# Optimization experiments

Measured on AMD Instinct MI355X. Metric: run time of the kernel, lower is better.

The kernel has to match this reference:

```python
import jax, jax.numpy as jnp
import numpy as np

EPS = 1.1920929e-07  # torch RMSNorm default eps = float32 finfo eps

def rms_norm(x, w):
    return x * jax.lax.rsqrt(jnp.mean(x * x, axis=-1, keepdims=True) + EPS) * w

def setup_inputs() -> dict:
    key = jax.random.key(0)
    ks = jax.random.split(key, 10)
    B, C, H, W = 8, 64, 48, 48
    E = C  # embed_dim = query_dim = key_dim = value_dim
    q = jax.random.normal(ks[0], (B, C, H, W), jnp.float32)
    k = jax.random.normal(ks[1], (B, C, H, W), jnp.float32)
    v = jax.random.normal(ks[2], (B, C, H, W), jnp.float32)
    s = 1.0 / np.sqrt(E)
    conv_w = jax.random.normal(ks[3], (C, C, 3, 3), jnp.float32) * (1.0 / np.sqrt(C * 9))
    nq_w = jnp.ones((E,), jnp.float32)
    nk_w = jnp.ones((E,), jnp.float32)
    wq = jax.random.normal(ks[4], (E, E), jnp.float32) * s
    bq = jax.random.normal(ks[5], (E,), jnp.float32) * 0.01
    wk = jax.random.normal(ks[6], (E, E), jnp.float32) * s
    bk = jax.random.normal(ks[7], (E,), jnp.float32) * 0.01
    return {"q": q, "k": k, "v": v, "conv_w": conv_w, "nq_w": nq_w,
            "nk_w": nk_w, "wq": wq, "bq": bq, "wk": wk, "bk": bk}

def reference(q, k, v, conv_w, nq_w, nk_w, wq, bq, wk, bk):
    B, C, H, W = q.shape
    num_heads = 4
    head_dim = C // num_heads
    # conv2d 3x3, stride 1, same padding, no bias
    qc = jax.lax.conv_general_dilated(
        q, conv_w, window_strides=(1, 1), padding='SAME',
        dimension_numbers=('NCHW', 'OIHW', 'NCHW'))
    # b c h w -> b (h w) c
    qs = qc.reshape(B, C, H * W).transpose(0, 2, 1)
    ksq = k.reshape(B, C, -1).transpose(0, 2, 1)
    vsq = v.reshape(B, C, -1).transpose(0, 2, 1)
    # RMSNorm on q and k (norm_v output feeds MHA value path whose output is discarded)
    qn = rms_norm(qs, nq_w)
    kn = rms_norm(ksq, nk_w)
    # MHA projections (q scaled by 1/sqrt(head_dim) as in torch)
    qp = (qn @ wq.T + bq) * (1.0 / np.sqrt(head_dim))
    kp = ksq_p = kn @ wk.T + bk
    Sq, Sk = qp.shape[1], kp.shape[1]
    qh = qp.reshape(B, Sq, num_heads, head_dim)
    kh = kp.reshape(B, Sk, num_heads, head_dim)
    scores = jnp.einsum('bihd,bjhd->bhij', qh, kh)
    attn = jax.nn.softmax(scores, axis=-1)
    # average_attn_weights=True -> mean over heads
    attn_avg = jnp.mean(attn, axis=1)  # [b, i, j]
    # custom output: weighted sum over RAW (un-normed, unprojected) value
    out = jnp.einsum('bij,bjd->bid', attn_avg, vsq)
    return out
```

## Files before the change

### kernel.cpp

```cpp
#include <hip/hip_runtime.h>
#include <hip/hip_bf16.h>

namespace {
constexpr int kB = 8;
constexpr int kC = 64;
constexpr int kH = 48;
constexpr int kW = 48;
constexpr int kS = kH * kW;
constexpr float kEps = 1.1920929e-07f;
constexpr float kQScale = 0.25f * 1.4426950408889634f;
}

typedef __attribute__((ext_vector_type(8))) short short8;
typedef __attribute__((ext_vector_type(4))) float f32x4;

__device__ __forceinline__ short f2bf(float x) {
  unsigned u = __float_as_uint(x);
  u += 0x7fffu + ((u >> 16) & 1u);
  return (short)(u >> 16);
}
__device__ __forceinline__ float bf2f(short s) {
  return __uint_as_float(((unsigned)(unsigned short)s) << 16);
}
__device__ __forceinline__ float fexp2(float x) {
  return __builtin_amdgcn_exp2f(x);
}

__global__ __launch_bounds__(256) void fused_prep(
    const float* __restrict__ q, const float* __restrict__ k,
    const float* __restrict__ v, const float* __restrict__ wq,
    const float* __restrict__ wk, const float* __restrict__ conv_w,
    short* __restrict__ qt, short* __restrict__ kt, short* __restrict__ vq,
    short* __restrict__ wqb3, short* __restrict__ wkb3, short* __restrict__ wt3) {
  const int blk = blockIdx.x;
  if (blk < 576) {
    __shared__ float tile[64][65];
    const int zz = blk / 36;
    const int bx = blk % 36;
    const int b = zz >> 1;
    const float* src = (zz & 1) ? k : q;
    short* dst = (zz & 1) ? kt : qt;
    const int s0 = bx * 64;
    const int tx = threadIdx.x & 63;
    const int ty = threadIdx.x >> 6;
#pragma unroll
    for (int r = 0; r < 16; ++r) {
      int c = r * 4 + ty;
      tile[c][tx] = src[((size_t)b * kC + c) * kS + s0 + tx];
    }
    __syncthreads();
#pragma unroll
    for (int r = 0; r < 16; ++r) {
      int s = r * 4 + ty;
      dst[((size_t)b * kS + s0 + s) * kC + tx] = f2bf(tile[tx][s]);
    }
  } else if (blk < 1152) {
    int g = (blk - 576) * 256 + threadIdx.x;
    int bb = g / 18432;
    int rem = g - bb * 18432;
    int jseg = rem >> 8;
    int sub = rem & 255;
    int d = sub >> 6;
    int Lq = sub & 63;
    const float* src = v + ((size_t)(bb * 64 + d * 16 + (Lq & 15))) * kS
                         + jseg * 32 + (Lq >> 4) * 8;
    float4 x0 = *reinterpret_cast<const float4*>(src);
    float4 x1 = *reinterpret_cast<const float4*>(src + 4);
    short8 o;
    o[0] = f2bf(x0.x); o[1] = f2bf(x0.y); o[2] = f2bf(x0.z); o[3] = f2bf(x0.w);
    o[4] = f2bf(x1.x); o[5] = f2bf(x1.y); o[6] = f2bf(x1.z); o[7] = f2bf(x1.w);
    *reinterpret_cast<short8*>(vq + (size_t)g * 8) = o;
  } else {
    int idx = (blk - 1152) * 256 + threadIdx.x;
    if (idx < 4096) {
      int j = idx & 7, Lw = (idx >> 3) & 63, slab = idx >> 9;
      int nt = slab & 3, kh = slab >> 2;
      int e = nt * 16 + (Lw & 15), c = kh * 32 + (Lw >> 4) * 8 + j;
      wqb3[idx] = f2bf(wq[e * 64 + c]);
    } else if (idx < 8192) {
      int i2 = idx - 4096;
      int j = i2 & 7, Lw = (i2 >> 3) & 63, slab = i2 >> 9;
      int nt = slab & 3, kh = slab >> 2;
      int e = nt * 16 + (Lw & 15), c = kh * 32 + (Lw >> 4) * 8 + j;
      wkb3[i2] = f2bf(wk[e * 64 + c]);
    } else {
      int i3 = idx - 8192;
      int j = i3 & 7, Lw = (i3 >> 3) & 63, slab = i3 >> 9;
      int nt = slab & 3, kh = (slab >> 2) & 1, tap = slab >> 3;
      int co = nt * 16 + (Lw & 15), ci = kh * 32 + (Lw >> 4) * 8 + j;
      wt3[i3] = f2bf(conv_w[co * 576 + ci * 9 + tap]);
    }
  }
}

__global__ __launch_bounds__(256) void fused_qk_gemm(
    const short* __restrict__ qt, const short* __restrict__ kt,
    const short* __restrict__ wt3, const short* __restrict__ wqb3,
    const short* __restrict__ wkb3,
    const float* __restrict__ nq_w, const float* __restrict__ nk_w,
    const float* __restrict__ bq, const float* __restrict__ bk,
    short* __restrict__ qp, short* __restrict__ kq) {
  __shared__ __align__(16) short Qs[164][72];
  __shared__ __align__(16) short ln[4][16][80];
  const int blk = blockIdx.x;
  const int t = threadIdx.x;
  const int ws = t >> 6;
  const int L = t & 63;
  const int quad = L >> 4;
  const int l16 = L & 15;
  const short8 zero8 = {0, 0, 0, 0, 0, 0, 0, 0};

  if (blk < 288) {
    const int b = blk / 36;
    const int S0 = (blk % 36) * 64;
    const int sBase = S0 + ws * 16;
    const int s = sBase + l16;
    const int h = s / kW, w = s % kW;

    const short* qtb = qt + (size_t)b * kS * kC;
#pragma unroll
    for (int it = 0; it < 6; ++it) {
      int idx = it * 256 + t;
      if (idx < 164 * 8) {
        int r = idx >> 3, sg = idx & 7;
        int srow = S0 - 49 + r;
        srow = srow < 0 ? 0 : (srow >= kS ? kS - 1 : srow);
        *reinterpret_cast<int4*>(&Qs[r][sg * 8]) =
            *reinterpret_cast<const int4*>(qtb + (size_t)srow * kC + sg * 8);
      }
    }
    __syncthreads();

    const int baseLocal = ws * 16 + l16 + 49;
    f32x4 acc[4] = {{0.f, 0.f, 0.f, 0.f}, {0.f, 0.f, 0.f, 0.f},
                    {0.f, 0.f, 0.f, 0.f}, {0.f, 0.f, 0.f, 0.f}};
#pragma unroll
    for (int tap = 0; tap < 9; ++tap) {
      const int dh = tap / 3 - 1, dw = tap % 3 - 1;
      const bool valid = (unsigned)(h + dh) < (unsigned)kH &&
                         (unsigned)(w + dw) < (unsigned)kW;
      const int local = baseLocal + dh * kW + dw;
#pragma unroll
      for (int kh = 0; kh < 2; ++kh) {
        short8 af = *reinterpret_cast<const short8*>(&Qs[local][kh * 32 + quad * 8]);
        af = valid ? af : zero8;
        const short* wb = wt3 + ((tap * 2 + kh) * 4) * 512 + L * 8;
#pragma unroll
        for (int nt = 0; nt < 4; ++nt) {
          short8 bf = *reinterpret_cast<const short8*>(wb + nt * 512);
          acc[nt] = __builtin_amdgcn_mfma_f32_16x16x32_bf16(af, bf, acc[nt], 0, 0, 0);
        }
      }
    }
    float rstd[4];
#pragma unroll
    for (int reg = 0; reg < 4; ++reg) {
      float pr = acc[0][reg] * acc[0][reg] + acc[1][reg] * acc[1][reg]
               + acc[2][reg] * acc[2][reg] + acc[3][reg] * acc[3][reg];
      pr += __shfl_xor(pr, 1, 64);
      pr += __shfl_xor(pr, 2, 64);
      pr += __shfl_xor(pr, 4, 64);
      pr += __shfl_xor(pr, 8, 64);
      rstd[reg] = rsqrtf(pr * (1.0f / kC) + kEps);
    }
#pragma unroll
    for (int nt = 0; nt < 4; ++nt) {
      float g = nq_w[nt * 16 + l16];
#pragma unroll
      for (int reg = 0; reg < 4; ++reg) {
        ln[ws][quad * 4 + reg][nt * 16 + l16] = f2bf(acc[nt][reg] * rstd[reg] * g);
      }
    }
    __syncthreads();
    f32x4 acc2[4] = {{0.f, 0.f, 0.f, 0.f}, {0.f, 0.f, 0.f, 0.f},
                     {0.f, 0.f, 0.f, 0.f}, {0.f, 0.f, 0.f, 0.f}};
#pragma unroll
    for (int kh = 0; kh < 2; ++kh) {
      short8 af = *reinterpret_cast<const short8*>(&ln[ws][l16][kh * 32 + quad * 8]);
      const short* wb = wqb3 + (kh * 4) * 512 + L * 8;
#pragma unroll
      for (int nt = 0; nt < 4; ++nt) {
        short8 bf = *reinterpret_cast<const short8*>(wb + nt * 512);
        acc2[nt] = __builtin_amdgcn_mfma_f32_16x16x32_bf16(af, bf, acc2[nt], 0, 0, 0);
      }
    }
#pragma unroll
    for (int nt = 0; nt < 4; ++nt) {
      const int e = nt * 16 + l16;
      float bias = bq[e];
#pragma unroll
      for (int reg = 0; reg < 4; ++reg) {
        qp[((size_t)b * kS + sBase + quad * 4 + reg) * kC + e] =
            f2bf((acc2[nt][reg] + bias) * kQScale);
      }
    }
  } else {
    const int idx = blk - 288;
    const int b = idx / 36;
    const int S0 = (idx % 36) * 64;
    const int sBase = S0 + ws * 16;

    const short* ktb = kt + ((size_t)b * kS + S0) * kC;
#pragma unroll
    for (int it = 0; it < 2; ++it) {
      int r = it * 32 + (t >> 3), sg = t & 7;
      *reinterpret_cast<int4*>(&Qs[r][sg * 8]) =
          *reinterpret_cast<const int4*>(ktb + (size_t)r * kC + sg * 8);
    }
    __syncthreads();

    short8 af0 = *reinterpret_cast<const short8*>(&Qs[ws * 16 + l16][quad * 8]);
    short8 af1 = *reinterpret_cast<const short8*>(&Qs[ws * 16 + l16][32 + quad * 8]);

    float xs[16];
#pragma unroll
    for (int j = 0; j < 8; ++j) { xs[j] = bf2f(af0[j]); xs[8 + j] = bf2f(af1[j]); }
    float sum = 0.f;
#pragma unroll
    for (int j = 0; j < 16; ++j) sum = fmaf(xs[j], xs[j], sum);
    sum += __shfl_xor(sum, 16, 64);
    sum += __shfl_xor(sum, 32, 64);
    float rstd = rsqrtf(sum * (1.0f / kC) + kEps);

    const float* n0 = nk_w + quad * 8;
#pragma unroll
    for (int j = 0; j < 8; ++j) {
      af0[j] = f2bf(xs[j] * rstd * n0[j]);
      af1[j] = f2bf(xs[8 + j] * rstd * n0[32 + j]);
    }

    f32x4 acc[4] = {{0.f, 0.f, 0.f, 0.f}, {0.f, 0.f, 0.f, 0.f},
                    {0.f, 0.f, 0.f, 0.f}, {0.f, 0.f, 0.f, 0.f}};
#pragma unroll
    for (int nt = 0; nt < 4; ++nt) {
      short8 bf0 = *reinterpret_cast<const short8*>(
          wkb3 + (0 * 4 + nt) * 512 + L * 8);
      short8 bf1 = *reinterpret_cast<const short8*>(
          wkb3 + (1 * 4 + nt) * 512 + L * 8);
      acc[nt] = __builtin_amdgcn_mfma_f32_16x16x32_bf16(af0, bf0, acc[nt], 0, 0, 0);
      acc[nt] = __builtin_amdgcn_mfma_f32_16x16x32_bf16(af1, bf1, acc[nt], 0, 0, 0);
    }
    short* kqb = kq + (size_t)b * 147456;
#pragma unroll
    for (int nt = 0; nt < 4; ++nt) {
      const int e = nt * 16 + l16;
      const int hp = nt >> 1;
      const int quadp = ((nt & 1) << 1) | (l16 >> 3);
      const int elem = l16 & 7;
      float bias = bk[e];
#pragma unroll
      for (int reg = 0; reg < 4; ++reg) {
        int s = sBase + quad * 4 + reg;
        int jseg = s >> 5, jrow = s & 31;
        int c = (jrow >> 2) & 1;
        int l16p = ((jrow >> 3) << 2) | (jrow & 3);
        kqb[((((size_t)jseg * 2 + hp) * 2 + c) * 64 + quadp * 16 + l16p) * 8 + elem] =
            f2bf(acc[nt][reg] + bias);
      }
    }
  }
}

#define LOADT(K0, K1, V0, V1, V2, V3, JT)                                      \
  do {                                                                         \
    const short* kb_ = kbase + (size_t)(JT) * 4096;                            \
    const short* vb_ = vbase + (size_t)(JT) * 4096;                            \
    K0 = *reinterpret_cast<const short8*>(kb_);                                \
    K1 = *reinterpret_cast<const short8*>(kb_ + 512);                          \
    V0 = *reinterpret_cast<const short8*>(vb_);                                \
    V1 = *reinterpret_cast<const short8*>(vb_ + 512);                          \
    V2 = *reinterpret_cast<const short8*>(vb_ + 1024);                         \
    V3 = *reinterpret_cast<const short8*>(vb_ + 1536);                         \
  } while (0)

#define PHASE(K0, K1, V0, V1, V2, V3)                                          \
  do {                                                                         \
    _Pragma("unroll")                                                          \
    for (int hl = 0; hl < 2; ++hl) {                                           \
      f32x4 s0 = __builtin_amdgcn_mfma_f32_16x16x32_bf16(K0, qm[hl], zc, 0, 0, 0); \
      f32x4 s1 = __builtin_amdgcn_mfma_f32_16x16x32_bf16(K1, qm[hl], zc, 0, 0, 0); \
      float e0 = fexp2(s0[0]), e1 = fexp2(s0[1]);                              \
      float e2 = fexp2(s0[2]), e3 = fexp2(s0[3]);                              \
      float f0 = fexp2(s1[0]), f1 = fexp2(s1[1]);                              \
      float f2 = fexp2(s1[2]), f3 = fexp2(s1[3]);                              \
      union { __hip_bfloat162 h2[4]; short8 s8; } cv;                          \
      cv.h2[0] = __float22bfloat162_rn(make_float2(e0, e1));                   \
      cv.h2[1] = __float22bfloat162_rn(make_float2(e2, e3));                   \
      cv.h2[2] = __float22bfloat162_rn(make_float2(f0, f1));                   \
      cv.h2[3] = __float22bfloat162_rn(make_float2(f2, f3));                   \
      U[hl][0] = __builtin_amdgcn_mfma_f32_16x16x32_bf16(V0, cv.s8, U[hl][0], 0, 0, 0); \
      U[hl][1] = __builtin_amdgcn_mfma_f32_16x16x32_bf16(V1, cv.s8, U[hl][1], 0, 0, 0); \
      U[hl][2] = __builtin_amdgcn_mfma_f32_16x16x32_bf16(V2, cv.s8, U[hl][2], 0, 0, 0); \
      U[hl][3] = __builtin_amdgcn_mfma_f32_16x16x32_bf16(V3, cv.s8, U[hl][3], 0, 0, 0); \
      Ul[hl]   = __builtin_amdgcn_mfma_f32_16x16x32_bf16(af_l, cv.s8, Ul[hl], 0, 0, 0); \
    }                                                                          \
  } while (0)

__global__ __launch_bounds__(256, 4) void attn_flash(
    const short* __restrict__ qp, const short* __restrict__ kq,
    const short* __restrict__ vq, float* __restrict__ out) {
  __shared__ float pl[4][16][2];
  __shared__ float Li[32][2];
  __shared__ __align__(16) float slab[16][66];

  const int blk = blockIdx.x;
  const int b = blk & 7;
  const int idx = blk >> 3;
  const int hp = idx & 1;
  const int i0 = (idx >> 1) * 32;
  const int t = threadIdx.x;
  const int ws = t >> 6;
  const int isub = ws & 1;
  const int jhalf = ws >> 1;
  const int L = t & 63;
  const int quad = L >> 4;
  const int l16 = L & 15;

  const f32x4 zc = {0.f, 0.f, 0.f, 0.f};
  const short8 z8 = {0, 0, 0, 0, 0, 0, 0, 0};
  const short ob = (short)0x3F80;
  const short8 ones8 = {ob, ob, ob, ob, ob, ob, ob, ob};
  const short8 af_l = (l16 == 0) ? ones8 : z8;

  const short* qrow = qp + ((size_t)b * kS + i0 + isub * 16 + l16) * kC + hp * 32;
  const short8 qw = *reinterpret_cast<const short8*>(qrow + quad * 8);
  const bool lo = quad < 2;
  const short8 qm[2] = {lo ? qw : z8, lo ? z8 : qw};

  const short* kbase =
      kq + (((size_t)(b * 72 + jhalf) * 2 + hp) * 2 * 64 + L) * 8;
  const short* vbase = vq + ((size_t)(b * 72 + jhalf) * 4 * 64 + L) * 8;

  f32x4 U[2][4];
#pragma unroll
  for (int hl = 0; hl < 2; ++hl)
#pragma unroll
    for (int d = 0; d < 4; ++d) U[hl][d] = zc;
  f32x4 Ul[2] = {zc, zc};

  short8 ka0, ka1, va0, va1, va2, va3;
  short8 kb0, kb1, vb0, vb1, vb2, vb3;
  LOADT(ka0, ka1, va0, va1, va2, va3, 0);
  LOADT(kb0, kb1, vb0, vb1, vb2, vb3, 1);

  for (int jt = 0; jt < 34; jt += 2) {
    PHASE(ka0, ka1, va0, va1, va2, va3);
    LOADT(ka0, ka1, va0, va1, va2, va3, jt + 2);
    PHASE(kb0, kb1, vb0, vb1, vb2, vb3);
    LOADT(kb0, kb1, vb0, vb1, vb2, vb3, jt + 3);
  }
  PHASE(ka0, ka1, va0, va1, va2, va3);
  PHASE(kb0, kb1, vb0, vb1, vb2, vb3);

  if (quad == 0) {
#pragma unroll
    for (int hl = 0; hl < 2; ++hl) pl[ws][l16][hl] = Ul[hl][0];
  }
  __syncthreads();
  if (t < 64) {
    const int i = t >> 1, h2 = t & 1;
    Li[i][h2] = 0.25f / (pl[i >> 4][i & 15][h2] + pl[(i >> 4) + 2][i & 15][h2]);
  }
  __syncthreads();
  float c2[2];
#pragma unroll
  for (int hl = 0; hl < 2; ++hl) c2[hl] = Li[isub * 16 + l16][hl];

#pragma unroll
  for (int d = 0; d < 4; ++d) {
    if (jhalf == 1) {
#pragma unroll
      for (int hl = 0; hl < 2; ++hl)
#pragma unroll
        for (int reg = 0; reg < 4; ++reg)
          slab[(isub * 2 + hl) * 4 + reg][L] = U[hl][d][reg];
    }
    __syncthreads();
    if (jhalf == 0) {
      float of[4] = {0.f, 0.f, 0.f, 0.f};
#pragma unroll
      for (int hl = 0; hl < 2; ++hl) {
#pragma unroll
        for (int reg = 0; reg < 4; ++reg) {
          float tot = U[hl][d][reg] + slab[(isub * 2 + hl) * 4 + reg][L];
          of[reg] += tot * c2[hl];
        }
      }
      float* op = out + ((size_t)b * kS + i0 + isub * 16 + l16) * kC + d * 16 + quad * 4;
#pragma unroll
      for (int reg = 0; reg < 4; ++reg) atomicAdd(op + reg, of[reg]);
    }
    __syncthreads();
  }
}

extern "C" void kernel_launch(void* const* d_in, const int* in_sizes, int n_in,
                              void* d_out, int out_size, void* d_ws, size_t ws_size,
                              hipStream_t stream) {
  const float* q      = (const float*)d_in[0];
  const float* k      = (const float*)d_in[1];
  const float* v      = (const float*)d_in[2];
  const float* conv_w = (const float*)d_in[3];
  const float* nq_w   = (const float*)d_in[4];
  const float* nk_w   = (const float*)d_in[5];
  const float* wq     = (const float*)d_in[6];
  const float* bq     = (const float*)d_in[7];
  const float* wk     = (const float*)d_in[8];
  const float* bk     = (const float*)d_in[9];
  float* out = (float*)d_out;

  const size_t N = (size_t)kB * kS * kC;
  short* qt   = (short*)d_ws;
  short* kt   = qt + N;
  short* vq   = kt + N;
  short* qp   = vq + N;
  short* kq   = qp + N;
  short* wqb3 = kq + N;
  short* wkb3 = wqb3 + 4096;
  short* wt3  = wkb3 + 4096;

  hipMemsetAsync(d_out, 0, out_size, stream);

  fused_prep<<<1328, 256, 0, stream>>>(q, k, v, wq, wk, conv_w,
                                       qt, kt, vq, wqb3, wkb3, wt3);
  fused_qk_gemm<<<576, 256, 0, stream>>>(qt, kt, wt3, wqb3, wkb3,
                                         nq_w, nk_w, bq, bk, qp, kq);
  attn_flash<<<1152, 256, 0, stream>>>(qp, kq, vq, out);
}
```

Baseline: 148.6 us.

## Fuse q/k transpose into QK GEMM kernel and fold output memset into prep

The q and k NCHW-to-token-major bf16 transposes move out of the prep kernel and into the QK GEMM kernel, which now reads fp32 q/k directly and transposes them through shared memory. This removes the qt/kt intermediate buffers and their global round trip. The hipMemsetAsync on the output is replaced by extra blocks in the prep kernel, dropping one launch. In exchange, the conv blocks reload a 164-row halo in three transpose passes with extra barriers, so the halo rows are read redundantly across neighbouring blocks.

```diff
diff --git a/kernel.cpp b/kernel.cpp
--- a/kernel.cpp
+++ b/kernel.cpp
@@ -26,36 +26,15 @@
   return __builtin_amdgcn_exp2f(x);
 }
 
-__global__ __launch_bounds__(256) void fused_prep(
-    const float* __restrict__ q, const float* __restrict__ k,
+__global__ __launch_bounds__(256) void prep_lite(
     const float* __restrict__ v, const float* __restrict__ wq,
     const float* __restrict__ wk, const float* __restrict__ conv_w,
-    short* __restrict__ qt, short* __restrict__ kt, short* __restrict__ vq,
-    short* __restrict__ wqb3, short* __restrict__ wkb3, short* __restrict__ wt3) {
+    short* __restrict__ vq, short* __restrict__ wqb3, short* __restrict__ wkb3,
+    short* __restrict__ wt3, float* __restrict__ out) {
   const int blk = blockIdx.x;
+  const int t = threadIdx.x;
   if (blk < 576) {
-    __shared__ float tile[64][65];
-    const int zz = blk / 36;
-    const int bx = blk % 36;
-    const int b = zz >> 1;
-    const float* src = (zz & 1) ? k : q;
-    short* dst = (zz & 1) ? kt : qt;
-    const int s0 = bx * 64;
-    const int tx = threadIdx.x & 63;
-    const int ty = threadIdx.x >> 6;
-#pragma unroll
-    for (int r = 0; r < 16; ++r) {
-      int c = r * 4 + ty;
-      tile[c][tx] = src[((size_t)b * kC + c) * kS + s0 + tx];
-    }
-    __syncthreads();
-#pragma unroll
-    for (int r = 0; r < 16; ++r) {
-      int s = r * 4 + ty;
-      dst[((size_t)b * kS + s0 + s) * kC + tx] = f2bf(tile[tx][s]);
-    }
-  } else if (blk < 1152) {
-    int g = (blk - 576) * 256 + threadIdx.x;
+    int g = blk * 256 + t;
     int bb = g / 18432;
     int rem = g - bb * 18432;
     int jseg = rem >> 8;
@@ -70,8 +49,8 @@
     o[0] = f2bf(x0.x); o[1] = f2bf(x0.y); o[2] = f2bf(x0.z); o[3] = f2bf(x0.w);
     o[4] = f2bf(x1.x); o[5] = f2bf(x1.y); o[6] = f2bf(x1.z); o[7] = f2bf(x1.w);
     *reinterpret_cast<short8*>(vq + (size_t)g * 8) = o;
-  } else {
-    int idx = (blk - 1152) * 256 + threadIdx.x;
+  } else if (blk < 752) {
+    int idx = (blk - 576) * 256 + t;
     if (idx < 4096) {
       int j = idx & 7, Lw = (idx >> 3) & 63, slab = idx >> 9;
       int nt = slab & 3, kh = slab >> 2;
@@ -90,11 +69,16 @@
       int co = nt * 16 + (Lw & 15), ci = kh * 32 + (Lw >> 4) * 8 + j;
       wt3[i3] = f2bf(conv_w[co * 576 + ci * 9 + tap]);
     }
-  }
-}
-
-__global__ __launch_bounds__(256) void fused_qk_gemm(
-    const short* __restrict__ qt, const short* __restrict__ kt,
+  } else {
+    size_t i = (size_t)(blk - 752) * 256 + t;
+    float4 z = make_float4(0.f, 0.f, 0.f, 0.f);
+    *reinterpret_cast<float4*>(out + i * 8) = z;
+    *reinterpret_cast<float4*>(out + i * 8 + 4) = z;
+  }
+}
+
+__global__ __launch_bounds__(256) void qk_gemm_t(
+    const float* __restrict__ q, const float* __restrict__ k,
     const short* __restrict__ wt3, const short* __restrict__ wqb3,
     const short* __restrict__ wkb3,
     const float* __restrict__ nq_w, const float* __restrict__ nk_w,
@@ -102,12 +86,15 @@
     short* __restrict__ qp, short* __restrict__ kq) {
   __shared__ __align__(16) short Qs[164][72];
   __shared__ __align__(16) short ln[4][16][80];
+  __shared__ float tile[64][65];
   const int blk = blockIdx.x;
   const int t = threadIdx.x;
   const int ws = t >> 6;
   const int L = t & 63;
   const int quad = L >> 4;
   const int l16 = L & 15;
+  const int tx = t & 63;
+  const int ty = t >> 6;
   const short8 zero8 = {0, 0, 0, 0, 0, 0, 0, 0};
 
   if (blk < 288) {
@@ -117,19 +104,25 @@
     const int s = sBase + l16;
     const int h = s / kW, w = s % kW;
 
-    const short* qtb = qt + (size_t)b * kS * kC;
-#pragma unroll
-    for (int it = 0; it < 6; ++it) {
-      int idx = it * 256 + t;
-      if (idx < 164 * 8) {
-        int r = idx >> 3, sg = idx & 7;
-        int srow = S0 - 49 + r;
-        srow = srow < 0 ? 0 : (srow >= kS ? kS - 1 : srow);
-        *reinterpret_cast<int4*>(&Qs[r][sg * 8]) =
-            *reinterpret_cast<const int4*>(qtb + (size_t)srow * kC + sg * 8);
-      }
-    }
-    __syncthreads();
+    const float* qb = q + (size_t)b * kC * kS;
+#pragma unroll
+    for (int p = 0; p < 3; ++p) {
+      int scol = S0 - 49 + p * 64 + tx;
+      scol = scol < 0 ? 0 : (scol >= kS ? kS - 1 : scol);
+#pragma unroll
+      for (int r = 0; r < 16; ++r) {
+        int c = r * 4 + ty;
+        tile[c][tx] = qb[(size_t)c * kS + scol];
+      }
+      __syncthreads();
+#pragma unroll
+      for (int r = 0; r < 16; ++r) {
+        int j = r * 4 + ty;
+        int srow = p * 64 + j;
+        if (srow < 164) Qs[srow][tx] = f2bf(tile[tx][j]);
+      }
+      __syncthreads();
+    }
 
     const int baseLocal = ws * 16 + l16 + 49;
     f32x4 acc[4] = {{0.f, 0.f, 0.f, 0.f}, {0.f, 0.f, 0.f, 0.f},
@@ -200,12 +193,17 @@
     const int S0 = (idx % 36) * 64;
     const int sBase = S0 + ws * 16;
 
-    const short* ktb = kt + ((size_t)b * kS + S0) * kC;
-#pragma unroll
-    for (int it = 0; it < 2; ++it) {
-      int r = it * 32 + (t >> 3), sg = t & 7;
-      *reinterpret_cast<int4*>(&Qs[r][sg * 8]) =
-          *reinterpret_cast<const int4*>(ktb + (size_t)r * kC + sg * 8);
+    const float* kb = k + (size_t)b * kC * kS;
+#pragma unroll
+    for (int r = 0; r < 16; ++r) {
+      int c = r * 4 + ty;
+      tile[c][tx] = kb[(size_t)c * kS + S0 + tx];
+    }
+    __syncthreads();
+#pragma unroll
+    for (int r = 0; r < 16; ++r) {
+      int j = r * 4 + ty;
+      Qs[j][tx] = f2bf(tile[tx][j]);
     }
     __syncthreads();
 
@@ -243,11 +241,10 @@
     short* kqb = kq + (size_t)b * 147456;
 #pragma unroll
     for (int nt = 0; nt < 4; ++nt) {
-      const int e = nt * 16 + l16;
       const int hp = nt >> 1;
       const int quadp = ((nt & 1) << 1) | (l16 >> 3);
       const int elem = l16 & 7;
-      float bias = bk[e];
+      float bias = bk[nt * 16 + l16];
 #pragma unroll
       for (int reg = 0; reg < 4; ++reg) {
         int s = sBase + quad * 4 + reg;
@@ -410,20 +407,16 @@
   float* out = (float*)d_out;
 
   const size_t N = (size_t)kB * kS * kC;
-  short* qt   = (short*)d_ws;
-  short* kt   = qt + N;
-  short* vq   = kt + N;
+  short* vq   = (short*)d_ws;
   short* qp   = vq + N;
   short* kq   = qp + N;
   short* wqb3 = kq + N;
   short* wkb3 = wqb3 + 4096;
   short* wt3  = wkb3 + 4096;
 
-  hipMemsetAsync(d_out, 0, out_size, stream);
-
-  fused_prep<<<1328, 256, 0, stream>>>(q, k, v, wq, wk, conv_w,
-                                       qt, kt, vq, wqb3, wkb3, wt3);
-  fused_qk_gemm<<<576, 256, 0, stream>>>(qt, kt, wt3, wqb3, wkb3,
-                                         nq_w, nk_w, bq, bk, qp, kq);
+  prep_lite<<<1328, 256, 0, stream>>>(v, wq, wk, conv_w,
+                                      vq, wqb3, wkb3, wt3, out);
+  qk_gemm_t<<<576, 256, 0, stream>>>(q, k, wt3, wqb3, wkb3,
+                                     nq_w, nk_w, bq, bk, qp, kq);
   attn_flash<<<1152, 256, 0, stream>>>(qp, kq, vq, out);
 }
```

Measured after the change: 144.0 us. 3.1% less time.
